# Kernel optimization log

Hardware: AMD Instinct MI355X
Metric: run time of the kernel (lower is better)

Reference implementation:

```python
import jax, jax.numpy as jnp
import numpy as np

N, D_IN, F = 65536, 512, 256
E = 524288
BATCH, K1 = 32, 200
BN_EPS = 1e-5


def setup_inputs() -> dict:
    key = jax.random.key(0)
    ks = iter(jax.random.split(key, 64))

    def nrm(shape, s=0.05):
        return jax.random.normal(next(ks), shape, jnp.float32) * s

    inp = {
        "feat": jax.random.normal(next(ks), (N, D_IN), jnp.float32),
        "A": jax.random.randint(next(ks), (2, E), 0, N, dtype=jnp.int32),
        "h1id": jax.random.randint(next(ks), (BATCH * K1,), 0, N // BATCH, dtype=jnp.int32),
        "batch": BATCH,
    }
    dims = [(D_IN, F), (F, F), (F, F), (F, F)]
    for i, (di, do) in enumerate(dims, 1):
        inp[f"eps{i}"] = jnp.zeros((), jnp.float32)          # GINConv train_eps, init 0
        inp[f"w{i}a"] = nrm((di, do)); inp[f"b{i}a"] = jnp.zeros((do,), jnp.float32)
        inp[f"w{i}b"] = nrm((do, do)); inp[f"b{i}b"] = jnp.zeros((do,), jnp.float32)
        inp[f"g{i}"] = jnp.ones((do,), jnp.float32)          # BN gamma
        inp[f"be{i}"] = jnp.zeros((do,), jnp.float32)        # BN beta
        inp[f"m{i}"] = nrm((do,))                            # BN running mean
        inp[f"v{i}"] = jax.random.uniform(next(ks), (do,), jnp.float32, 0.5, 1.5)  # BN running var
    inp["wc1"] = nrm((F, F)); inp["bc1"] = jnp.zeros((F,), jnp.float32)
    inp["pa"] = jnp.full((F,), 0.25, jnp.float32)            # PReLU per-channel slope
    inp["wc2"] = nrm((F, 2)); inp["bc2"] = jnp.zeros((2,), jnp.float32)
    return inp


def _gin_conv(x, src, dst, eps, wa, ba, wb, bb, g, be, m, v):
    # sum aggregation over in-edges: aggr[i] = sum_{(j->i)} x[j]
    aggr = jax.ops.segment_sum(x[src], dst, num_segments=N)
    h = (1.0 + eps) * x + aggr
    h = jax.nn.relu(h @ wa + ba) @ wb + bb
    # BatchNorm1d in eval mode (running stats)
    return (h - m) * jax.lax.rsqrt(v + BN_EPS) * g + be


def _forward(feat, A, h1id, batch,
             eps1, w1a, b1a, w1b, b1b, g1, be1, m1, v1,
             eps2, w2a, b2a, w2b, b2b, g2, be2, m2, v2,
             eps3, w3a, b3a, w3b, b3b, g3, be3, m3, v3,
             eps4, w4a, b4a, w4b, b4b, g4, be4, m4, v4,
             wc1, bc1, pa, wc2, bc2):
    src, dst = A[0], A[1]
    h = jax.nn.relu(_gin_conv(feat, src, dst, eps1, w1a, b1a, w1b, b1b, g1, be1, m1, v1))
    h = jax.nn.relu(_gin_conv(h, src, dst, eps2, w2a, b2a, w2b, b2b, g2, be2, m2, v2))
    h = jax.nn.relu(_gin_conv(h, src, dst, eps3, w3a, b3a, w3b, b3b, g3, be3, m3, v3))
    h = _gin_conv(h, src, dst, eps4, w4a, b4a, w4b, b4b, g4, be4, m4, v4)
    score = h.reshape(batch, -1, F)                      # [B, n_per_graph, F]
    idx = h1id.reshape(batch, K1)
    edge_feat = jnp.take_along_axis(score, idx[:, :, None], axis=1)  # [B, K1, F]
    ef = edge_feat.reshape(-1, F)
    hc = ef @ wc1 + bc1
    hc = jnp.where(hc > 0, hc, pa * hc)                  # PReLU(256)
    return hc @ wc2 + bc2                                # [B*K1, 2]


def reference(feat, A, h1id, batch,
              eps1, w1a, b1a, w1b, b1b, g1, be1, m1, v1,
              eps2, w2a, b2a, w2b, b2b, g2, be2, m2, v2,
              eps3, w3a, b3a, w3b, b3b, g3, be3, m3, v3,
              eps4, w4a, b4a, w4b, b4b, g4, be4, m4, v4,
              wc1, bc1, pa, wc2, bc2):
    return _forward(feat, A, h1id, batch,
                    eps1, w1a, b1a, w1b, b1b, g1, be1, m1, v1,
                    eps2, w2a, b2a, w2b, b2b, g2, be2, m2, v2,
                    eps3, w3a, b3a, w3b, b3b, g3, be3, m3, v3,
                    eps4, w4a, b4a, w4b, b4b, g4, be4, m4, v4,
                    wc1, bc1, pa, wc2, bc2)
```

## Files before the change

kernel.cpp:

```cpp
#include <hip/hip_runtime.h>

typedef unsigned short u16;
typedef unsigned int   u32;
typedef __bf16  bf16x8 __attribute__((ext_vector_type(8)));
typedef float   f32x4  __attribute__((ext_vector_type(4)));
typedef u32     u32x4  __attribute__((ext_vector_type(4)));

#define NN 65536
#define NE 524288
#define FD 256

typedef const __attribute__((address_space(1))) void* gas_p;
typedef __attribute__((address_space(3))) void* las_p;
#define GLDS16(g, l) __builtin_amdgcn_global_load_lds((gas_p)(const void*)(g), (las_p)(void*)(l), 16, 0, 0)

__device__ __forceinline__ u16 f2bf(float f){
  u32 u = __float_as_uint(f);
  u += 0x7fffu + ((u >> 16) & 1u);
  return (u16)(u >> 16);
}
__device__ __forceinline__ float bf2f(u32 lo16){
  return __uint_as_float(lo16 << 16);
}
__device__ __forceinline__ void acc8(float* a, uint4 v){
  a[0] += bf2f(v.x & 0xffffu); a[1] += bf2f(v.x >> 16);
  a[2] += bf2f(v.y & 0xffffu); a[3] += bf2f(v.y >> 16);
  a[4] += bf2f(v.z & 0xffffu); a[5] += bf2f(v.z >> 16);
  a[6] += bf2f(v.w & 0xffffu); a[7] += bf2f(v.w >> 16);
}

__global__ __launch_bounds__(256) void prep_k(
    const float* __restrict__ w1a, const float* __restrict__ w1b,
    const float* __restrict__ w2a, const float* __restrict__ w2b,
    const float* __restrict__ w3a, const float* __restrict__ w3b,
    const float* __restrict__ w4a, const float* __restrict__ w4b,
    const float* __restrict__ wc1, u16* __restrict__ wT)
{
  int idx = blockIdx.x * 256 + threadIdx.x;
  const float* src; int base, K, local;
  if (idx < 131072){ src = w1a; base = 0; K = 512; local = idx; }
  else {
    local = idx - 131072;
    int j = local >> 16;
    local &= 65535;
    K = 256;
    base = 131072 + j * 65536;
    switch (j){
      case 0: src = w1b; break;
      case 1: src = w2a; break;
      case 2: src = w2b; break;
      case 3: src = w3a; break;
      case 4: src = w3b; break;
      case 5: src = w4a; break;
      case 6: src = w4b; break;
      default: src = wc1; break;
    }
  }
  int n = local & 255;
  int k = local >> 8;
  wT[base + n * K + k] = f2bf(src[k * 256 + n]);
}

__global__ __launch_bounds__(256) void hist_k(const int* __restrict__ dst, int* __restrict__ deg){
  int e = blockIdx.x * 256 + threadIdx.x;
  atomicAdd(&deg[dst[e]], 1);
}

__global__ __launch_bounds__(1024) void scan_k(const int* __restrict__ deg, int* __restrict__ rs){
  __shared__ int part[1024];
  int t = threadIdx.x;
  int base = t * 64;
  int sum = 0;
  for (int i = 0; i < 64; ++i) sum += deg[base + i];
  part[t] = sum;
  __syncthreads();
  for (int off = 1; off < 1024; off <<= 1){
    int v = 0;
    if (t >= off) v = part[t - off];
    __syncthreads();
    part[t] += v;
    __syncthreads();
  }
  int run = part[t] - sum;
  for (int i = 0; i < 64; ++i){ rs[base + i] = run; run += deg[base + i]; }
  if (t == 1023) rs[65536] = part[1023];
}

__global__ __launch_bounds__(256) void scat_k(
    const int* __restrict__ src, const int* __restrict__ dst,
    const int* __restrict__ rs, int* __restrict__ cursor, int* __restrict__ csr)
{
  int e = blockIdx.x * 256 + threadIdx.x;
  int d = dst[e];
  int pos = atomicAdd(&cursor[d], 1);
  csr[rs[d] + pos] = src[e];
}

template<int AF32, int MODE, int RELU, int K>
__global__ __launch_bounds__(512) void gemm_k(
    const void* __restrict__ Ap, const u16* __restrict__ Bt,
    u16* __restrict__ C,
    const float* __restrict__ p0, const float* __restrict__ p1,
    const float* __restrict__ p2, const float* __restrict__ p3,
    const float* __restrict__ p4)
{
  __shared__ u16 lds[32768];
  u16* As = lds;
  u16* Bs = lds + 8192;
  const int t    = threadIdx.x;
  const int lane = t & 63;
  const int w    = t >> 6;
  const int wm   = w & 1;
  const int wn   = w >> 1;
  const int m0   = blockIdx.x * 128;
  const int mrow = lane & 15;
  const int quad = lane >> 4;

  f32x4 acc[4][4];
  const f32x4 zero = {0.f, 0.f, 0.f, 0.f};
  #pragma unroll
  for (int i = 0; i < 4; ++i)
    #pragma unroll
    for (int j = 0; j < 4; ++j) acc[i][j] = zero;

  const u16* Ab = (const u16*)Ap;
  const float* Af = (const float*)Ap;

  for (int k0 = 0; k0 < K; k0 += 64){
    if (AF32){
      #pragma unroll
      for (int i = 0; i < 2; ++i){
        int p   = i * 512 + t;
        int row = p >> 3;
        const float* s = Af + (size_t)(m0 + row) * K + k0 + (p & 7) * 8;
        float4 x0 = *(const float4*)s;
        float4 x1 = *(const float4*)(s + 4);
        union { u32x4 q; u16 h[8]; } u;
        u.h[0] = f2bf(x0.x); u.h[1] = f2bf(x0.y); u.h[2] = f2bf(x0.z); u.h[3] = f2bf(x0.w);
        u.h[4] = f2bf(x1.x); u.h[5] = f2bf(x1.y); u.h[6] = f2bf(x1.z); u.h[7] = f2bf(x1.w);
        int dst = (p & ~7) | ((p & 7) ^ (row & 7));
        *(u32x4*)&As[dst * 8] = u.q;
      }
    } else {
      #pragma unroll
      for (int i = 0; i < 2; ++i){
        int p   = i * 512 + t;
        int row = p >> 3;
        int ch  = (p & 7) ^ (row & 7);
        GLDS16(Ab + (size_t)(m0 + row) * K + k0 + ch * 8, &As[p * 8]);
      }
    }
    #pragma unroll
    for (int i = 0; i < 4; ++i){
      int p   = i * 512 + t;
      int row = p >> 3;
      int ch  = (p & 7) ^ (row & 7);
      GLDS16(Bt + (size_t)row * K + k0 + ch * 8, &Bs[p * 8]);
    }
    __syncthreads();
    #pragma unroll
    for (int ks = 0; ks < 2; ++ks){
      bf16x8 af[4], bq[4];
      #pragma unroll
      for (int mi = 0; mi < 4; ++mi){
        int r  = wm * 64 + mi * 16 + mrow;
        int ch = (quad + ks * 4) ^ (r & 7);
        af[mi] = *(const bf16x8*)&As[(r * 8 + ch) * 8];
      }
      #pragma unroll
      for (int ni = 0; ni < 4; ++ni){
        int rb = wn * 64 + ni * 16 + mrow;
        int ch = (quad + ks * 4) ^ (rb & 7);
        bq[ni] = *(const bf16x8*)&Bs[(rb * 8 + ch) * 8];
      }
      #pragma unroll
      for (int mi = 0; mi < 4; ++mi)
        #pragma unroll
        for (int ni = 0; ni < 4; ++ni)
          acc[mi][ni] = __builtin_amdgcn_mfma_f32_16x16x32_bf16(af[mi], bq[ni], acc[mi][ni], 0, 0, 0);
    }
    __syncthreads();
  }

  #pragma unroll
  for (int ni = 0; ni < 4; ++ni){
    int c  = wn * 64 + ni * 16 + mrow;
    float scale = 1.f, shift = 0.f, slope = 0.f;
    if (MODE == 1){
      float s = p0[c] * rsqrtf(p3[c] + 1e-5f);
      scale = s;
      shift = (p4[c] - p2[c]) * s + p1[c];
    }
    if (MODE == 2){ shift = p0[c]; slope = p1[c]; }
    #pragma unroll
    for (int mi = 0; mi < 4; ++mi){
      int rbase = wm * 64 + mi * 16 + quad * 4;
      #pragma unroll
      for (int reg = 0; reg < 4; ++reg){
        float v = acc[mi][ni][reg];
        if (MODE == 1){
          v = v * scale + shift;
          if (RELU) v = fmaxf(v, 0.f);
        }
        if (MODE == 2){
          v += shift;
          v = v > 0.f ? v : slope * v;
        }
        lds[(rbase + reg) * 256 + c] = f2bf(v);
      }
    }
  }
  __syncthreads();
  #pragma unroll
  for (int i = 0; i < 8; ++i){
    int p  = i * 512 + t;
    int r  = p >> 5;
    int ch = p & 31;
    u32x4 q = *(const u32x4*)&lds[r * 256 + ch * 8];
    *(u32x4*)&C[(size_t)(m0 + r) * 256 + ch * 8] = q;
  }
}

template<int GATH>
__global__ __launch_bounds__(256) void agg_k(
    const u16* __restrict__ y, const int* __restrict__ rs, const int* __restrict__ csr,
    const float* __restrict__ epsp, const float* __restrict__ bias,
    const int* __restrict__ gidx, u16* __restrict__ tout)
{
  int sub    = threadIdx.x >> 5;
  int lane32 = threadIdx.x & 31;
  int idx    = blockIdx.x * 8 + sub;
  int node;
  if (GATH) node = (idx / 200) * 2048 + gidx[idx];
  else      node = idx;
  int f0 = lane32 * 8;
  float e1 = 1.0f + epsp[0];
  int s0 = rs[node], s1 = rs[node + 1];
  float a[8] = {0.f,0.f,0.f,0.f,0.f,0.f,0.f,0.f};
  int e = s0;
  for (; e + 4 <= s1; e += 4){
    int sa = csr[e], sb = csr[e+1], sc = csr[e+2], sd = csr[e+3];
    uint4 va = *(const uint4*)(y + (size_t)sa * 256 + f0);
    uint4 vb = *(const uint4*)(y + (size_t)sb * 256 + f0);
    uint4 vc = *(const uint4*)(y + (size_t)sc * 256 + f0);
    uint4 vd = *(const uint4*)(y + (size_t)sd * 256 + f0);
    acc8(a, va); acc8(a, vb); acc8(a, vc); acc8(a, vd);
  }
  for (; e < s1; ++e){
    int s = csr[e];
    acc8(a, *(const uint4*)(y + (size_t)s * 256 + f0));
  }
  uint4 own = *(const uint4*)(y + (size_t)node * 256 + f0);
  float ow[8];
  ow[0] = bf2f(own.x & 0xffffu); ow[1] = bf2f(own.x >> 16);
  ow[2] = bf2f(own.y & 0xffffu); ow[3] = bf2f(own.y >> 16);
  ow[4] = bf2f(own.z & 0xffffu); ow[5] = bf2f(own.z >> 16);
  ow[6] = bf2f(own.w & 0xffffu); ow[7] = bf2f(own.w >> 16);
  float4 b0 = *(const float4*)(bias + f0);
  float4 b1 = *(const float4*)(bias + f0 + 4);
  float r[8];
  r[0] = fmaxf(e1 * ow[0] + a[0] + b0.x, 0.f);
  r[1] = fmaxf(e1 * ow[1] + a[1] + b0.y, 0.f);
  r[2] = fmaxf(e1 * ow[2] + a[2] + b0.z, 0.f);
  r[3] = fmaxf(e1 * ow[3] + a[3] + b0.w, 0.f);
  r[4] = fmaxf(e1 * ow[4] + a[4] + b1.x, 0.f);
  r[5] = fmaxf(e1 * ow[5] + a[5] + b1.y, 0.f);
  r[6] = fmaxf(e1 * ow[6] + a[6] + b1.z, 0.f);
  r[7] = fmaxf(e1 * ow[7] + a[7] + b1.w, 0.f);
  uint4 o;
  o.x = (u32)f2bf(r[0]) | ((u32)f2bf(r[1]) << 16);
  o.y = (u32)f2bf(r[2]) | ((u32)f2bf(r[3]) << 16);
  o.z = (u32)f2bf(r[4]) | ((u32)f2bf(r[5]) << 16);
  o.w = (u32)f2bf(r[6]) | ((u32)f2bf(r[7]) << 16);
  *(uint4*)(tout + (size_t)idx * 256 + f0) = o;
}

__global__ __launch_bounds__(256) void head_k(
    const u16* __restrict__ hc, const float* __restrict__ wc2,
    const float* __restrict__ bc2, float* __restrict__ out)
{
  int row  = blockIdx.x * 4 + (threadIdx.x >> 6);
  int lane = threadIdx.x & 63;
  int f0   = lane * 4;
  uint2 hv = *(const uint2*)(hc + (size_t)row * 256 + f0);
  float h0 = bf2f(hv.x & 0xffffu), h1 = bf2f(hv.x >> 16);
  float h2 = bf2f(hv.y & 0xffffu), h3 = bf2f(hv.y >> 16);
  float4 wa = *(const float4*)(wc2 + f0 * 2);
  float4 wb = *(const float4*)(wc2 + f0 * 2 + 4);
  float acc0 = h0 * wa.x + h1 * wa.z + h2 * wb.x + h3 * wb.z;
  float acc1 = h0 * wa.y + h1 * wa.w + h2 * wb.y + h3 * wb.w;
  #pragma unroll
  for (int off = 32; off > 0; off >>= 1){
    acc0 += __shfl_xor(acc0, off);
    acc1 += __shfl_xor(acc1, off);
  }
  if (lane == 0){
    out[row * 2]     = acc0 + bc2[0];
    out[row * 2 + 1] = acc1 + bc2[1];
  }
}

extern "C" void kernel_launch(void* const* d_in, const int* in_sizes, int n_in,
                              void* d_out, int out_size, void* d_ws, size_t ws_size,
                              hipStream_t stream)
{
  const float* feat = (const float*)d_in[0];
  const int*   A    = (const int*)d_in[1];
  const int*   h1id = (const int*)d_in[2];
  const float* eps[4] = {(const float*)d_in[4],  (const float*)d_in[13], (const float*)d_in[22], (const float*)d_in[31]};
  const float* wa [4] = {(const float*)d_in[5],  (const float*)d_in[14], (const float*)d_in[23], (const float*)d_in[32]};
  const float* ba [4] = {(const float*)d_in[6],  (const float*)d_in[15], (const float*)d_in[24], (const float*)d_in[33]};
  const float* wb [4] = {(const float*)d_in[7],  (const float*)d_in[16], (const float*)d_in[25], (const float*)d_in[34]};
  const float* bb [4] = {(const float*)d_in[8],  (const float*)d_in[17], (const float*)d_in[26], (const float*)d_in[35]};
  const float* g  [4] = {(const float*)d_in[9],  (const float*)d_in[18], (const float*)d_in[27], (const float*)d_in[36]};
  const float* be [4] = {(const float*)d_in[10], (const float*)d_in[19], (const float*)d_in[28], (const float*)d_in[37]};
  const float* m  [4] = {(const float*)d_in[11], (const float*)d_in[20], (const float*)d_in[29], (const float*)d_in[38]};
  const float* v  [4] = {(const float*)d_in[12], (const float*)d_in[21], (const float*)d_in[30], (const float*)d_in[39]};
  const float* wc1 = (const float*)d_in[40];
  const float* bc1 = (const float*)d_in[41];
  const float* pa  = (const float*)d_in[42];
  const float* wc2 = (const float*)d_in[43];
  const float* bc2 = (const float*)d_in[44];

  char* ws = (char*)d_ws;
  u16* wT     = (u16*)(ws + 0);
  int* deg    = (int*)(ws + 1310720);
  int* rs     = (int*)(ws + 1572864);
  int* cursor = (int*)(ws + 1835264);
  int* csr    = (int*)(ws + 2097408);
  u16* ybuf   = (u16*)(ws + 4194560);
  u16* tbuf   = (u16*)(ws + 37748992);
  u16* hbuf   = (u16*)(ws + 71303424);
  u16* h4     = (u16*)(ws + 104857856);
  u16* hc     = (u16*)(ws + 108134656);

  u16* w1aT = wT;
  u16* w1bT = wT + 131072;
  u16* w2aT = wT + 196608;
  u16* w2bT = wT + 262144;
  u16* w3aT = wT + 327680;
  u16* w3bT = wT + 393216;
  u16* w4aT = wT + 458752;
  u16* w4bT = wT + 524288;
  u16* wc1T = wT + 589824;

  hipMemsetAsync(deg, 0, 65536 * 4, stream);
  hipMemsetAsync(cursor, 0, 65536 * 4, stream);
  prep_k<<<2560, 256, 0, stream>>>(wa[0], wb[0], wa[1], wb[1], wa[2], wb[2], wa[3], wb[3], wc1, wT);
  hist_k<<<NE / 256, 256, 0, stream>>>(A + NE, deg);
  scan_k<<<1, 1024, 0, stream>>>(deg, rs);
  scat_k<<<NE / 256, 256, 0, stream>>>(A, A + NE, rs, cursor, csr);

  const u16* waT[4] = {w1aT, w2aT, w3aT, w4aT};
  const u16* wbT[4] = {w1bT, w2bT, w3bT, w4bT};

  gemm_k<1,0,0,512><<<512, 512, 0, stream>>>(feat, waT[0], ybuf,
      nullptr, nullptr, nullptr, nullptr, nullptr);
  agg_k<0><<<NN / 8, 256, 0, stream>>>(ybuf, rs, csr, eps[0], ba[0], nullptr, tbuf);
  gemm_k<0,1,1,256><<<512, 512, 0, stream>>>(tbuf, wbT[0], hbuf,
      g[0], be[0], m[0], v[0], bb[0]);

  for (int l = 1; l <= 2; ++l){
    gemm_k<0,0,0,256><<<512, 512, 0, stream>>>(hbuf, waT[l], ybuf,
        nullptr, nullptr, nullptr, nullptr, nullptr);
    agg_k<0><<<NN / 8, 256, 0, stream>>>(ybuf, rs, csr, eps[l], ba[l], nullptr, tbuf);
    gemm_k<0,1,1,256><<<512, 512, 0, stream>>>(tbuf, wbT[l], hbuf,
        g[l], be[l], m[l], v[l], bb[l]);
  }

  gemm_k<0,0,0,256><<<512, 512, 0, stream>>>(hbuf, waT[3], ybuf,
      nullptr, nullptr, nullptr, nullptr, nullptr);
  agg_k<1><<<800, 256, 0, stream>>>(ybuf, rs, csr, eps[3], ba[3], h1id, tbuf);
  gemm_k<0,1,0,256><<<50, 512, 0, stream>>>(tbuf, wbT[3], h4,
      g[3], be[3], m[3], v[3], bb[3]);

  gemm_k<0,2,0,256><<<50, 512, 0, stream>>>(h4, wc1T, hc,
      bc1, pa, nullptr, nullptr, nullptr);
  head_k<<<1600, 256, 0, stream>>>(hc, wc2, bc2, (float*)d_out);

  (void)in_sizes; (void)n_in; (void)out_size; (void)ws_size;
}
```

Measured before the change: 636.0 us.

## Fuse aggregation, second MLP GEMM, BN and next-layer first GEMM per tile

Adds a fused kernel that, for each 128-row tile, gathers neighbour sums into LDS, runs the layer's second GEMM with BN+ReLU, then immediately runs the next layer's first GEMM and writes only that result. This replaces three launches per layer with one and avoids writing and re-reading the intermediate t and h buffers in global memory. In exchange, B operands are read straight from global memory without LDS staging, the gather phase may leave the matrix units idle, and the large LDS footprint limits occupancy.

```diff
diff --git a/kernel.cpp b/kernel.cpp
--- a/kernel.cpp
+++ b/kernel.cpp
@@ -218,6 +218,166 @@
     int ch = p & 31;
     u32x4 q = *(const u32x4*)&lds[r * 256 + ch * 8];
     *(u32x4*)&C[(size_t)(m0 + r) * 256 + ch * 8] = q;
+  }
+}
+
+__global__ __launch_bounds__(512) void fuse_k(
+    const u16* __restrict__ y, const int* __restrict__ rs, const int* __restrict__ csr,
+    const float* __restrict__ epsp, const float* __restrict__ abias,
+    const u16* __restrict__ B1t,
+    const float* __restrict__ g, const float* __restrict__ be,
+    const float* __restrict__ m, const float* __restrict__ v,
+    const float* __restrict__ bb,
+    const u16* __restrict__ B2t,
+    u16* __restrict__ yout)
+{
+  __shared__ u16 lds[32768];
+  const int t    = threadIdx.x;
+  const int lane = t & 63;
+  const int w    = t >> 6;
+  const int wm   = w & 1;
+  const int wn   = w >> 1;
+  const int m0   = blockIdx.x * 128;
+  const int mrow = lane & 15;
+  const int quad = lane >> 4;
+
+  {
+    int lane32 = lane & 31;
+    int half   = lane >> 5;
+    int f0     = lane32 * 8;
+    float e1 = 1.0f + epsp[0];
+    float4 b0 = *(const float4*)(abias + f0);
+    float4 b1 = *(const float4*)(abias + f0 + 4);
+    #pragma unroll 1
+    for (int i = 0; i < 8; ++i){
+      int r    = w * 16 + i * 2 + half;
+      int node = m0 + r;
+      int s0 = rs[node], s1 = rs[node + 1];
+      float a[8] = {0.f,0.f,0.f,0.f,0.f,0.f,0.f,0.f};
+      int e = s0;
+      for (; e + 4 <= s1; e += 4){
+        int sa = csr[e], sb = csr[e+1], sc = csr[e+2], sd = csr[e+3];
+        uint4 va = *(const uint4*)(y + (size_t)sa * 256 + f0);
+        uint4 vb = *(const uint4*)(y + (size_t)sb * 256 + f0);
+        uint4 vc = *(const uint4*)(y + (size_t)sc * 256 + f0);
+        uint4 vd = *(const uint4*)(y + (size_t)sd * 256 + f0);
+        acc8(a, va); acc8(a, vb); acc8(a, vc); acc8(a, vd);
+      }
+      for (; e < s1; ++e)
+        acc8(a, *(const uint4*)(y + (size_t)csr[e] * 256 + f0));
+      uint4 own = *(const uint4*)(y + (size_t)node * 256 + f0);
+      float r0 = fmaxf(e1 * bf2f(own.x & 0xffffu) + a[0] + b0.x, 0.f);
+      float r1 = fmaxf(e1 * bf2f(own.x >> 16)     + a[1] + b0.y, 0.f);
+      float r2 = fmaxf(e1 * bf2f(own.y & 0xffffu) + a[2] + b0.z, 0.f);
+      float r3 = fmaxf(e1 * bf2f(own.y >> 16)     + a[3] + b0.w, 0.f);
+      float r4 = fmaxf(e1 * bf2f(own.z & 0xffffu) + a[4] + b1.x, 0.f);
+      float r5 = fmaxf(e1 * bf2f(own.z >> 16)     + a[5] + b1.y, 0.f);
+      float r6 = fmaxf(e1 * bf2f(own.w & 0xffffu) + a[6] + b1.z, 0.f);
+      float r7 = fmaxf(e1 * bf2f(own.w >> 16)     + a[7] + b1.w, 0.f);
+      uint4 o;
+      o.x = (u32)f2bf(r0) | ((u32)f2bf(r1) << 16);
+      o.y = (u32)f2bf(r2) | ((u32)f2bf(r3) << 16);
+      o.z = (u32)f2bf(r4) | ((u32)f2bf(r5) << 16);
+      o.w = (u32)f2bf(r6) | ((u32)f2bf(r7) << 16);
+      int ch = lane32 ^ (r & 7);
+      *(uint4*)&lds[r * 256 + ch * 8] = o;
+    }
+  }
+  __syncthreads();
+
+  const f32x4 zero = {0.f, 0.f, 0.f, 0.f};
+
+  f32x4 acc[4][4];
+  #pragma unroll
+  for (int i = 0; i < 4; ++i)
+    #pragma unroll
+    for (int j = 0; j < 4; ++j) acc[i][j] = zero;
+  #pragma unroll
+  for (int ks = 0; ks < 8; ++ks){
+    bf16x8 af[4], bq[4];
+    #pragma unroll
+    for (int mi = 0; mi < 4; ++mi){
+      int r    = wm * 64 + mi * 16 + mrow;
+      int slot = (ks * 4 + quad) ^ (r & 7);
+      af[mi] = *(const bf16x8*)&lds[r * 256 + slot * 8];
+    }
+    #pragma unroll
+    for (int ni = 0; ni < 4; ++ni){
+      int rb = wn * 64 + ni * 16 + mrow;
+      bq[ni] = *(const bf16x8*)&B1t[(size_t)rb * 256 + ks * 32 + quad * 8];
+    }
+    #pragma unroll
+    for (int mi = 0; mi < 4; ++mi)
+      #pragma unroll
+      for (int ni = 0; ni < 4; ++ni)
+        acc[mi][ni] = __builtin_amdgcn_mfma_f32_16x16x32_bf16(af[mi], bq[ni], acc[mi][ni], 0, 0, 0);
+  }
+  __syncthreads();
+
+  #pragma unroll
+  for (int ni = 0; ni < 4; ++ni){
+    int c = wn * 64 + ni * 16 + mrow;
+    float scale = g[c] * rsqrtf(v[c] + 1e-5f);
+    float shift = (bb[c] - m[c]) * scale + be[c];
+    #pragma unroll
+    for (int mi = 0; mi < 4; ++mi){
+      int rbase = wm * 64 + mi * 16 + quad * 4;
+      #pragma unroll
+      for (int reg = 0; reg < 4; ++reg){
+        int row = rbase + reg;
+        float val = fmaxf(acc[mi][ni][reg] * scale + shift, 0.f);
+        lds[row * 256 + (((c >> 3) ^ (row & 7)) << 3) + (c & 7)] = f2bf(val);
+      }
+    }
+  }
+  __syncthreads();
+
+  f32x4 acc2[4][4];
+  #pragma unroll
+  for (int i = 0; i < 4; ++i)
+    #pragma unroll
+    for (int j = 0; j < 4; ++j) acc2[i][j] = zero;
+  #pragma unroll
+  for (int ks = 0; ks < 8; ++ks){
+    bf16x8 af[4], bq[4];
+    #pragma unroll
+    for (int mi = 0; mi < 4; ++mi){
+      int r    = wm * 64 + mi * 16 + mrow;
+      int slot = (ks * 4 + quad) ^ (r & 7);
+      af[mi] = *(const bf16x8*)&lds[r * 256 + slot * 8];
+    }
+    #pragma unroll
+    for (int ni = 0; ni < 4; ++ni){
+      int rb = wn * 64 + ni * 16 + mrow;
+      bq[ni] = *(const bf16x8*)&B2t[(size_t)rb * 256 + ks * 32 + quad * 8];
+    }
+    #pragma unroll
+    for (int mi = 0; mi < 4; ++mi)
+      #pragma unroll
+      for (int ni = 0; ni < 4; ++ni)
+        acc2[mi][ni] = __builtin_amdgcn_mfma_f32_16x16x32_bf16(af[mi], bq[ni], acc2[mi][ni], 0, 0, 0);
+  }
+  __syncthreads();
+
+  #pragma unroll
+  for (int ni = 0; ni < 4; ++ni){
+    int c = wn * 64 + ni * 16 + mrow;
+    #pragma unroll
+    for (int mi = 0; mi < 4; ++mi){
+      int rbase = wm * 64 + mi * 16 + quad * 4;
+      #pragma unroll
+      for (int reg = 0; reg < 4; ++reg)
+        lds[(rbase + reg) * 256 + c] = f2bf(acc2[mi][ni][reg]);
+    }
+  }
+  __syncthreads();
+  #pragma unroll
+  for (int i = 0; i < 8; ++i){
+    int p  = i * 512 + t;
+    int r  = p >> 5;
+    int ch = p & 31;
+    u32x4 q = *(const u32x4*)&lds[r * 256 + ch * 8];
+    *(u32x4*)&yout[(size_t)(m0 + r) * 256 + ch * 8] = q;
   }
 }
 
@@ -351,27 +511,18 @@
   scan_k<<<1, 1024, 0, stream>>>(deg, rs);
   scat_k<<<NE / 256, 256, 0, stream>>>(A, A + NE, rs, cursor, csr);
 
-  const u16* waT[4] = {w1aT, w2aT, w3aT, w4aT};
-  const u16* wbT[4] = {w1bT, w2bT, w3bT, w4bT};
-
-  gemm_k<1,0,0,512><<<512, 512, 0, stream>>>(feat, waT[0], ybuf,
+  gemm_k<1,0,0,512><<<512, 512, 0, stream>>>(feat, w1aT, ybuf,
       nullptr, nullptr, nullptr, nullptr, nullptr);
-  agg_k<0><<<NN / 8, 256, 0, stream>>>(ybuf, rs, csr, eps[0], ba[0], nullptr, tbuf);
-  gemm_k<0,1,1,256><<<512, 512, 0, stream>>>(tbuf, wbT[0], hbuf,
-      g[0], be[0], m[0], v[0], bb[0]);
-
-  for (int l = 1; l <= 2; ++l){
-    gemm_k<0,0,0,256><<<512, 512, 0, stream>>>(hbuf, waT[l], ybuf,
-        nullptr, nullptr, nullptr, nullptr, nullptr);
-    agg_k<0><<<NN / 8, 256, 0, stream>>>(ybuf, rs, csr, eps[l], ba[l], nullptr, tbuf);
-    gemm_k<0,1,1,256><<<512, 512, 0, stream>>>(tbuf, wbT[l], hbuf,
-        g[l], be[l], m[l], v[l], bb[l]);
-  }
-
-  gemm_k<0,0,0,256><<<512, 512, 0, stream>>>(hbuf, waT[3], ybuf,
-      nullptr, nullptr, nullptr, nullptr, nullptr);
-  agg_k<1><<<800, 256, 0, stream>>>(ybuf, rs, csr, eps[3], ba[3], h1id, tbuf);
-  gemm_k<0,1,0,256><<<50, 512, 0, stream>>>(tbuf, wbT[3], h4,
+
+  fuse_k<<<512, 512, 0, stream>>>(ybuf, rs, csr, eps[0], ba[0], w1bT,
+      g[0], be[0], m[0], v[0], bb[0], w2aT, tbuf);
+  fuse_k<<<512, 512, 0, stream>>>(tbuf, rs, csr, eps[1], ba[1], w2bT,
+      g[1], be[1], m[1], v[1], bb[1], w3aT, ybuf);
+  fuse_k<<<512, 512, 0, stream>>>(ybuf, rs, csr, eps[2], ba[2], w3bT,
+      g[2], be[2], m[2], v[2], bb[2], w4aT, tbuf);
+
+  agg_k<1><<<800, 256, 0, stream>>>(tbuf, rs, csr, eps[3], ba[3], h1id, hbuf);
+  gemm_k<0,1,0,256><<<50, 512, 0, stream>>>(hbuf, w4bT, h4,
       g[3], be[3], m[3], v[3], bb[3]);
 
   gemm_k<0,2,0,256><<<50, 512, 0, stream>>>(h4, wc1T, hc,
```

Result: slower. 715.1 us (+12.4%).

## Aggregate only selected nodes before layer-4 GEMM, swizzle LDS epilogue, fuse hist

Applied to the files above, without the earlier changes.

For the last GIN layer, the code now aggregates the raw layer-3 outputs only for the 6400 gathered nodes and then applies the w4a GEMM (new MODE 3 with bias+ReLU) on those rows. This replaces the full 65536-row w4a GEMM and follows from linearity of aggregation with respect to the matmul. It also XOR-swizzles the LDS layout of the GEMM epilogue to reduce bank conflicts, deepens the aggregation gather loop to 8 in-flight loads, and folds the degree histogram into the weight-prep launch. Rounding order changes slightly because aggregation now happens before the matmul in bf16.

```diff
diff --git a/kernel.cpp b/kernel.cpp
--- a/kernel.cpp
+++ b/kernel.cpp
@@ -28,14 +28,23 @@
   a[4] += bf2f(v.z & 0xffffu); a[5] += bf2f(v.z >> 16);
   a[6] += bf2f(v.w & 0xffffu); a[7] += bf2f(v.w >> 16);
 }
-
-__global__ __launch_bounds__(256) void prep_k(
+__device__ __forceinline__ int lsw(int row, int c){
+  return row * 256 + ((((c >> 3) ^ (row & 7)) << 3) | (c & 7));
+}
+
+__global__ __launch_bounds__(256) void prep_hist_k(
     const float* __restrict__ w1a, const float* __restrict__ w1b,
     const float* __restrict__ w2a, const float* __restrict__ w2b,
     const float* __restrict__ w3a, const float* __restrict__ w3b,
     const float* __restrict__ w4a, const float* __restrict__ w4b,
-    const float* __restrict__ wc1, u16* __restrict__ wT)
-{
+    const float* __restrict__ wc1, u16* __restrict__ wT,
+    const int* __restrict__ dst, int* __restrict__ deg)
+{
+  if (blockIdx.x >= 2560){
+    int e = (blockIdx.x - 2560) * 256 + threadIdx.x;
+    atomicAdd(&deg[dst[e]], 1);
+    return;
+  }
   int idx = blockIdx.x * 256 + threadIdx.x;
   const float* src; int base, K, local;
   if (idx < 131072){ src = w1a; base = 0; K = 512; local = idx; }
@@ -61,11 +70,6 @@
   wT[base + n * K + k] = f2bf(src[k * 256 + n]);
 }
 
-__global__ __launch_bounds__(256) void hist_k(const int* __restrict__ dst, int* __restrict__ deg){
-  int e = blockIdx.x * 256 + threadIdx.x;
-  atomicAdd(&deg[dst[e]], 1);
-}
-
 __global__ __launch_bounds__(1024) void scan_k(const int* __restrict__ deg, int* __restrict__ rs){
   __shared__ int part[1024];
   int t = threadIdx.x;
@@ -192,6 +196,7 @@
       shift = (p4[c] - p2[c]) * s + p1[c];
     }
     if (MODE == 2){ shift = p0[c]; slope = p1[c]; }
+    if (MODE == 3){ shift = p0[c]; }
     #pragma unroll
     for (int mi = 0; mi < 4; ++mi){
       int rbase = wm * 64 + mi * 16 + quad * 4;
@@ -206,7 +211,10 @@
           v += shift;
           v = v > 0.f ? v : slope * v;
         }
-        lds[(rbase + reg) * 256 + c] = f2bf(v);
+        if (MODE == 3){
+          v = fmaxf(v + shift, 0.f);
+        }
+        lds[lsw(rbase + reg, c)] = f2bf(v);
       }
     }
   }
@@ -216,12 +224,12 @@
     int p  = i * 512 + t;
     int r  = p >> 5;
     int ch = p & 31;
-    u32x4 q = *(const u32x4*)&lds[r * 256 + ch * 8];
+    u32x4 q = *(const u32x4*)&lds[r * 256 + (ch ^ (r & 7)) * 8];
     *(u32x4*)&C[(size_t)(m0 + r) * 256 + ch * 8] = q;
   }
 }
 
-template<int GATH>
+template<int GATH, int RAW>
 __global__ __launch_bounds__(256) void agg_k(
     const u16* __restrict__ y, const int* __restrict__ rs, const int* __restrict__ csr,
     const float* __restrict__ epsp, const float* __restrict__ bias,
@@ -236,8 +244,19 @@
   int f0 = lane32 * 8;
   float e1 = 1.0f + epsp[0];
   int s0 = rs[node], s1 = rs[node + 1];
+  uint4 own = *(const uint4*)(y + (size_t)node * 256 + f0);
   float a[8] = {0.f,0.f,0.f,0.f,0.f,0.f,0.f,0.f};
   int e = s0;
+  for (; e + 8 <= s1; e += 8){
+    int si[8];
+    #pragma unroll
+    for (int q = 0; q < 8; ++q) si[q] = csr[e + q];
+    uint4 vv[8];
+    #pragma unroll
+    for (int q = 0; q < 8; ++q) vv[q] = *(const uint4*)(y + (size_t)si[q] * 256 + f0);
+    #pragma unroll
+    for (int q = 0; q < 8; ++q) acc8(a, vv[q]);
+  }
   for (; e + 4 <= s1; e += 4){
     int sa = csr[e], sb = csr[e+1], sc = csr[e+2], sd = csr[e+3];
     uint4 va = *(const uint4*)(y + (size_t)sa * 256 + f0);
@@ -250,23 +269,27 @@
     int s = csr[e];
     acc8(a, *(const uint4*)(y + (size_t)s * 256 + f0));
   }
-  uint4 own = *(const uint4*)(y + (size_t)node * 256 + f0);
   float ow[8];
   ow[0] = bf2f(own.x & 0xffffu); ow[1] = bf2f(own.x >> 16);
   ow[2] = bf2f(own.y & 0xffffu); ow[3] = bf2f(own.y >> 16);
   ow[4] = bf2f(own.z & 0xffffu); ow[5] = bf2f(own.z >> 16);
   ow[6] = bf2f(own.w & 0xffffu); ow[7] = bf2f(own.w >> 16);
-  float4 b0 = *(const float4*)(bias + f0);
-  float4 b1 = *(const float4*)(bias + f0 + 4);
   float r[8];
-  r[0] = fmaxf(e1 * ow[0] + a[0] + b0.x, 0.f);
-  r[1] = fmaxf(e1 * ow[1] + a[1] + b0.y, 0.f);
-  r[2] = fmaxf(e1 * ow[2] + a[2] + b0.z, 0.f);
-  r[3] = fmaxf(e1 * ow[3] + a[3] + b0.w, 0.f);
-  r[4] = fmaxf(e1 * ow[4] + a[4] + b1.x, 0.f);
-  r[5] = fmaxf(e1 * ow[5] + a[5] + b1.y, 0.f);
-  r[6] = fmaxf(e1 * ow[6] + a[6] + b1.z, 0.f);
-  r[7] = fmaxf(e1 * ow[7] + a[7] + b1.w, 0.f);
+  if (RAW){
+    #pragma unroll
+    for (int q = 0; q < 8; ++q) r[q] = e1 * ow[q] + a[q];
+  } else {
+    float4 b0 = *(const float4*)(bias + f0);
+    float4 b1 = *(const float4*)(bias + f0 + 4);
+    r[0] = fmaxf(e1 * ow[0] + a[0] + b0.x, 0.f);
+    r[1] = fmaxf(e1 * ow[1] + a[1] + b0.y, 0.f);
+    r[2] = fmaxf(e1 * ow[2] + a[2] + b0.z, 0.f);
+    r[3] = fmaxf(e1 * ow[3] + a[3] + b0.w, 0.f);
+    r[4] = fmaxf(e1 * ow[4] + a[4] + b1.x, 0.f);
+    r[5] = fmaxf(e1 * ow[5] + a[5] + b1.y, 0.f);
+    r[6] = fmaxf(e1 * ow[6] + a[6] + b1.z, 0.f);
+    r[7] = fmaxf(e1 * ow[7] + a[7] + b1.w, 0.f);
+  }
   uint4 o;
   o.x = (u32)f2bf(r[0]) | ((u32)f2bf(r[1]) << 16);
   o.y = (u32)f2bf(r[2]) | ((u32)f2bf(r[3]) << 16);
@@ -331,8 +354,10 @@
   u16* ybuf   = (u16*)(ws + 4194560);
   u16* tbuf   = (u16*)(ws + 37748992);
   u16* hbuf   = (u16*)(ws + 71303424);
-  u16* h4     = (u16*)(ws + 104857856);
-  u16* hc     = (u16*)(ws + 108134656);
+  u16* u4     = (u16*)(ws + 104857856);
+  u16* z4     = (u16*)(ws + 108134656);
+  u16* h4b    = (u16*)(ws + 111411456);
+  u16* hcb    = (u16*)(ws + 114688256);
 
   u16* w1aT = wT;
   u16* w1bT = wT + 131072;
@@ -346,37 +371,36 @@
 
   hipMemsetAsync(deg, 0, 65536 * 4, stream);
   hipMemsetAsync(cursor, 0, 65536 * 4, stream);
-  prep_k<<<2560, 256, 0, stream>>>(wa[0], wb[0], wa[1], wb[1], wa[2], wb[2], wa[3], wb[3], wc1, wT);
-  hist_k<<<NE / 256, 256, 0, stream>>>(A + NE, deg);
+  prep_hist_k<<<4608, 256, 0, stream>>>(wa[0], wb[0], wa[1], wb[1], wa[2], wb[2],
+      wa[3], wb[3], wc1, wT, A + NE, deg);
   scan_k<<<1, 1024, 0, stream>>>(deg, rs);
   scat_k<<<NE / 256, 256, 0, stream>>>(A, A + NE, rs, cursor, csr);
 
-  const u16* waT[4] = {w1aT, w2aT, w3aT, w4aT};
-  const u16* wbT[4] = {w1bT, w2bT, w3bT, w4bT};
-
-  gemm_k<1,0,0,512><<<512, 512, 0, stream>>>(feat, waT[0], ybuf,
+  gemm_k<1,0,0,512><<<512, 512, 0, stream>>>(feat, w1aT, ybuf,
       nullptr, nullptr, nullptr, nullptr, nullptr);
-  agg_k<0><<<NN / 8, 256, 0, stream>>>(ybuf, rs, csr, eps[0], ba[0], nullptr, tbuf);
-  gemm_k<0,1,1,256><<<512, 512, 0, stream>>>(tbuf, wbT[0], hbuf,
+  agg_k<0,0><<<NN / 8, 256, 0, stream>>>(ybuf, rs, csr, eps[0], ba[0], nullptr, tbuf);
+  gemm_k<0,1,1,256><<<512, 512, 0, stream>>>(tbuf, w1bT, hbuf,
       g[0], be[0], m[0], v[0], bb[0]);
 
   for (int l = 1; l <= 2; ++l){
-    gemm_k<0,0,0,256><<<512, 512, 0, stream>>>(hbuf, waT[l], ybuf,
+    const u16* waT = (l == 1) ? w2aT : w3aT;
+    const u16* wbT = (l == 1) ? w2bT : w3bT;
+    gemm_k<0,0,0,256><<<512, 512, 0, stream>>>(hbuf, waT, ybuf,
         nullptr, nullptr, nullptr, nullptr, nullptr);
-    agg_k<0><<<NN / 8, 256, 0, stream>>>(ybuf, rs, csr, eps[l], ba[l], nullptr, tbuf);
-    gemm_k<0,1,1,256><<<512, 512, 0, stream>>>(tbuf, wbT[l], hbuf,
+    agg_k<0,0><<<NN / 8, 256, 0, stream>>>(ybuf, rs, csr, eps[l], ba[l], nullptr, tbuf);
+    gemm_k<0,1,1,256><<<512, 512, 0, stream>>>(tbuf, wbT, hbuf,
         g[l], be[l], m[l], v[l], bb[l]);
   }
 
-  gemm_k<0,0,0,256><<<512, 512, 0, stream>>>(hbuf, waT[3], ybuf,
-      nullptr, nullptr, nullptr, nullptr, nullptr);
-  agg_k<1><<<800, 256, 0, stream>>>(ybuf, rs, csr, eps[3], ba[3], h1id, tbuf);
-  gemm_k<0,1,0,256><<<50, 512, 0, stream>>>(tbuf, wbT[3], h4,
+  agg_k<1,1><<<800, 256, 0, stream>>>(hbuf, rs, csr, eps[3], nullptr, h1id, u4);
+  gemm_k<0,3,0,256><<<50, 512, 0, stream>>>(u4, w4aT, z4,
+      ba[3], nullptr, nullptr, nullptr, nullptr);
+  gemm_k<0,1,0,256><<<50, 512, 0, stream>>>(z4, w4bT, h4b,
       g[3], be[3], m[3], v[3], bb[3]);
 
-  gemm_k<0,2,0,256><<<50, 512, 0, stream>>>(h4, wc1T, hc,
+  gemm_k<0,2,0,256><<<50, 512, 0, stream>>>(h4b, wc1T, hcb,
       bc1, pa, nullptr, nullptr, nullptr);
-  head_k<<<1600, 256, 0, stream>>>(hc, wc2, bc2, (float*)d_out);
+  head_k<<<1600, 256, 0, stream>>>(hcb, wc2, bc2, (float*)d_out);
 
   (void)in_sizes; (void)n_in; (void)out_size; (void)ws_size;
 }
```

Measured after the change: 642.4 us. Within noise of the previous version (+1.0%).
